# Kernel tuning notes

Measured on AMD Instinct MI355X. Metric: run time of the kernel, lower is better.

Reference implementation:

```python
import jax, jax.numpy as jnp
import numpy as np

BS, LX, LY, D, H, DK = 2, 2048, 2048, 1024, 16, 64


def setup_inputs() -> dict:
    key = jax.random.key(0)
    ks = jax.random.split(key, 12)
    s = 1.0 / np.sqrt(D)
    return {
        "x": jax.random.normal(ks[0], (BS, LX, D), jnp.float32),
        "y": jax.random.normal(ks[1], (BS, LY, D), jnp.float32),
        "mask": jnp.zeros((BS, 1, LX, LY), jnp.float32),
        "Wq": jax.random.normal(ks[2], (D, H * DK), jnp.float32) * s,
        "bq": jnp.zeros((H * DK,), jnp.float32),
        "Wk": jax.random.normal(ks[3], (D, H * DK), jnp.float32) * s,
        "bk": jnp.zeros((H * DK,), jnp.float32),
        "Wv": jax.random.normal(ks[4], (D, H * DK), jnp.float32) * s,
        "bv": jnp.zeros((H * DK,), jnp.float32),
        "Wo": jax.random.normal(ks[5], (H * DK, D), jnp.float32) * s,
        "bo": jnp.zeros((D,), jnp.float32),
    }


def reference(x, y, mask, Wq, bq, Wk, bk, Wv, bv, Wo, bo):
    bs, lx, _ = x.shape
    ly = y.shape[1]
    norm = DK ** 0.5
    # projections -> (bs, len, H, DK)
    q = (x @ Wq + bq).reshape(bs, lx, H, DK)
    k = (y @ Wk + bk).reshape(bs, ly, H, DK)
    v = (y @ Wv + bv).reshape(bs, ly, H, DK)
    # scores: (bs, H, lx, ly)
    scores = jnp.einsum('bxhd,byhd->bhxy', q, k) / norm + mask
    attn = jax.nn.softmax(scores, axis=-1)
    # output: (bs, lx, H, DK) -> (bs, lx, H*DK)
    out = jnp.einsum('bhxy,byhd->bxhd', attn, v).reshape(bs, lx, H * DK)
    return out @ Wo + bo
```

## Files before the change

### kernel.cpp

```cpp
#include <hip/hip_runtime.h>
#include <hip/hip_bf16.h>


typedef __bf16 bf16;
typedef __bf16 bf16x4 __attribute__((ext_vector_type(4)));
typedef __bf16 bf16x8 __attribute__((ext_vector_type(8)));
typedef float floatx4 __attribute__((ext_vector_type(4)));

#define MFMA16(a, b, c) __builtin_amdgcn_mfma_f32_16x16x32_bf16(a, b, c, 0, 0, 0)

constexpr int BS = 2, LX = 2048, LY = 2048, D = 1024, H = 16, DK = 64;
constexpr int HD = H * DK;
constexpr float LOG2E = 1.4426950408889634f;

__device__ __forceinline__ void cp16(const bf16* g, bf16* l) {
  __builtin_amdgcn_global_load_lds(
      (const __attribute__((address_space(1))) unsigned int*)g,
      (__attribute__((address_space(3))) unsigned int*)l, 16, 0, 0);
}

__global__ __launch_bounds__(256) void prep(const float* __restrict__ W0, bf16* __restrict__ T0,
                                            const float* __restrict__ W1, bf16* __restrict__ T1,
                                            const float* __restrict__ W2, bf16* __restrict__ T2,
                                            const float* __restrict__ W3, bf16* __restrict__ T3,
                                            const float* __restrict__ x, bf16* __restrict__ xb,
                                            const float* __restrict__ y, bf16* __restrict__ yb,
                                            const float* __restrict__ mask, int* __restrict__ flags) {
  const int id = blockIdx.x;
  const int t = threadIdx.x;
  if (id < 1024) {
    __shared__ bf16 tile[64][72];
    const float* W;
    bf16* T;
    switch (id >> 8) {
      case 0: W = W0; T = T0; break;
      case 1: W = W1; T = T1; break;
      case 2: W = W2; T = T2; break;
      default: W = W3; T = T3; break;
    }
    const int kt = id & 15, nt = (id >> 4) & 15;
    const int r = t >> 2, c4 = (t & 3) * 16;
    const float* src = W + (size_t)(kt * 64 + r) * 1024 + nt * 64 + c4;
#pragma unroll
    for (int i = 0; i < 16; i++) tile[r][c4 + i] = (bf16)src[i];
    __syncthreads();
    bf16 vals[16];
#pragma unroll
    for (int i = 0; i < 16; i++) vals[i] = tile[c4 + i][r];
    bf16* dst = T + (size_t)(nt * 64 + r) * 1024 + kt * 64 + c4;
#pragma unroll
    for (int i = 0; i < 16; i++) dst[i] = vals[i];
  } else if (id < 5120) {
    const int id2 = id - 1024;
    const float* src = (id2 >= 2048) ? y : x;
    bf16* dst = (id2 >= 2048) ? yb : xb;
    const size_t i = ((size_t)(id2 & 2047) * 256 + t) * 8;
    float4 a = *(const float4*)(src + i);
    float4 c = *(const float4*)(src + i + 4);
    bf16 tmp[8] = {(bf16)a.x, (bf16)a.y, (bf16)a.z, (bf16)a.w,
                   (bf16)c.x, (bf16)c.y, (bf16)c.z, (bf16)c.w};
    *(bf16x8*)(dst + i) = *(const bf16x8*)tmp;
  } else {
    const int id3 = id - 5120;
    const int region = id3 >> 5, sub = id3 & 31;
    const float4* p = (const float4*)mask + (size_t)region * 65536 + sub * 2048;
    bool nz = false;
#pragma unroll
    for (int it = 0; it < 8; it++) {
      float4 v = p[it * 256 + t];
      nz |= (v.x != 0.f) | (v.y != 0.f) | (v.z != 0.f) | (v.w != 0.f);
    }
    if (nz) atomicOr(&flags[region], 1);
  }
}

__global__ __launch_bounds__(256) void qkv_gemm(const bf16* __restrict__ xb, const bf16* __restrict__ yb,
                                                const bf16* __restrict__ Wtq, const bf16* __restrict__ Wtk,
                                                const bf16* __restrict__ Wtv,
                                                const float* __restrict__ bq, const float* __restrict__ bk,
                                                const float* __restrict__ bv,
                                                bf16* __restrict__ Qb, bf16* __restrict__ Kb,
                                                bf16* __restrict__ Vt) {
  constexpr int K = 1024, N = 1024;
  __shared__ __align__(16) bf16 smem[128 * 136];
  bf16* As = smem;
  bf16* Bs = smem + 128 * 64;
  bf16* Ct = smem;

  const int z = blockIdx.z;
  const bf16* A = (z == 0) ? xb : yb;
  const bf16* Bt = (z == 0) ? Wtq : (z == 1) ? Wtk : Wtv;
  const float* bias = (z == 0) ? bq : (z == 1) ? bk : bv;

  const int t = threadIdx.x;
  const int w = t >> 6, lane = t & 63, quad = lane >> 4, l15 = lane & 15;
  const int wr = (w & 1) * 64, wc = (w >> 1) * 64;
  const int mbase = blockIdx.y * 128, nbase = blockIdx.x * 128;
  const int srow = lane >> 3, schunk = (lane & 7) ^ srow;
  const int sx = quad ^ (l15 & 7);

  floatx4 acc[4][4] = {};

  for (int k0 = 0; k0 < K; k0 += 64) {
    __syncthreads();
#pragma unroll
    for (int j = 0; j < 4; j++) {
      const int r0 = w * 32 + j * 8;
      cp16(A + (size_t)(mbase + r0 + srow) * K + k0 + schunk * 8, As + r0 * 64);
      cp16(Bt + (size_t)(nbase + r0 + srow) * K + k0 + schunk * 8, Bs + r0 * 64);
    }
    __syncthreads();
    bf16x8 af[4][2], bfr[4][2];
#pragma unroll
    for (int i = 0; i < 4; i++) {
      const int ra = wr + i * 16 + l15;
      af[i][0] = *(const bf16x8*)&As[ra * 64 + sx * 8];
      af[i][1] = *(const bf16x8*)&As[ra * 64 + (sx ^ 4) * 8];
      const int rb = wc + i * 16 + l15;
      bfr[i][0] = *(const bf16x8*)&Bs[rb * 64 + sx * 8];
      bfr[i][1] = *(const bf16x8*)&Bs[rb * 64 + (sx ^ 4) * 8];
    }
#pragma unroll
    for (int i = 0; i < 4; i++)
#pragma unroll
      for (int jn = 0; jn < 4; jn++) {
        acc[i][jn] = MFMA16(af[i][0], bfr[jn][0], acc[i][jn]);
        acc[i][jn] = MFMA16(af[i][1], bfr[jn][1], acc[i][jn]);
      }
  }

  if (z <= 1) {
    bf16* outp = (z == 0) ? Qb : Kb;
    const float sc = (z == 0) ? 0.125f * LOG2E : 1.0f;
#pragma unroll
    for (int jn = 0; jn < 4; jn++) {
      const int n = nbase + wc + jn * 16 + l15;
      const float bv2 = bias[n];
#pragma unroll
      for (int i = 0; i < 4; i++)
#pragma unroll
        for (int r = 0; r < 4; r++) {
          const int m = mbase + wr + i * 16 + quad * 4 + r;
          outp[(size_t)m * N + n] = (bf16)((acc[i][jn][r] + bv2) * sc);
        }
    }
  } else {
    __syncthreads();
#pragma unroll
    for (int jn = 0; jn < 4; jn++) {
      const int nl = wc + jn * 16 + l15;
      const float bv2 = bias[nbase + nl];
#pragma unroll
      for (int i = 0; i < 4; i++)
#pragma unroll
        for (int r = 0; r < 4; r++) {
          const int ml = wr + i * 16 + quad * 4 + r;
          Ct[nl * 136 + ml] = (bf16)(acc[i][jn][r] + bv2);
        }
    }
    __syncthreads();
    const int n = t >> 1, mh = (t & 1) * 64;
    const int gn = nbase + n;
    const int hh = gn >> 6, dk = gn & 63;
    const int bb = mbase >> 11, y0 = (mbase & 2047) + mh;
    bf16* dst = Vt + ((size_t)(bb * H + hh) * DK + dk) * LY + y0;
    const bf16* srcr = &Ct[n * 136 + mh];
#pragma unroll
    for (int u = 0; u < 8; u++) *(bf16x8*)(dst + u * 8) = *(const bf16x8*)(srcr + u * 8);
  }
}

__global__ __launch_bounds__(256) void out_gemm(const bf16* __restrict__ A, const bf16* __restrict__ Bt,
                                                const float* __restrict__ bias, float* __restrict__ outp) {
  constexpr int K = 1024, N = 1024;
  __shared__ __align__(16) bf16 As[128 * 64];
  __shared__ __align__(16) bf16 Bs[64 * 64];
  const int t = threadIdx.x;
  const int w = t >> 6, lane = t & 63, quad = lane >> 4, l15 = lane & 15;
  const int mbase = blockIdx.y * 128, nbase = blockIdx.x * 64;
  const int srow = lane >> 3, schunk = (lane & 7) ^ srow;
  const int sx = quad ^ (l15 & 7);

  floatx4 acc[2][4] = {};
  for (int k0 = 0; k0 < K; k0 += 64) {
    __syncthreads();
#pragma unroll
    for (int j = 0; j < 4; j++) {
      const int r0 = w * 32 + j * 8;
      cp16(A + (size_t)(mbase + r0 + srow) * K + k0 + schunk * 8, As + r0 * 64);
    }
#pragma unroll
    for (int j = 0; j < 2; j++) {
      const int r0 = w * 16 + j * 8;
      cp16(Bt + (size_t)(nbase + r0 + srow) * K + k0 + schunk * 8, Bs + r0 * 64);
    }
    __syncthreads();
    bf16x8 af[2][2], bfr[4][2];
#pragma unroll
    for (int i = 0; i < 2; i++) {
      const int ra = w * 32 + i * 16 + l15;
      af[i][0] = *(const bf16x8*)&As[ra * 64 + sx * 8];
      af[i][1] = *(const bf16x8*)&As[ra * 64 + (sx ^ 4) * 8];
    }
#pragma unroll
    for (int jn = 0; jn < 4; jn++) {
      const int rb = jn * 16 + l15;
      bfr[jn][0] = *(const bf16x8*)&Bs[rb * 64 + sx * 8];
      bfr[jn][1] = *(const bf16x8*)&Bs[rb * 64 + (sx ^ 4) * 8];
    }
#pragma unroll
    for (int i = 0; i < 2; i++)
#pragma unroll
      for (int jn = 0; jn < 4; jn++) {
        acc[i][jn] = MFMA16(af[i][0], bfr[jn][0], acc[i][jn]);
        acc[i][jn] = MFMA16(af[i][1], bfr[jn][1], acc[i][jn]);
      }
  }
#pragma unroll
  for (int jn = 0; jn < 4; jn++) {
    const int n = nbase + jn * 16 + l15;
    const float bv2 = bias[n];
#pragma unroll
    for (int i = 0; i < 2; i++)
#pragma unroll
      for (int r = 0; r < 4; r++) {
        const int m = mbase + w * 32 + i * 16 + quad * 4 + r;
        outp[(size_t)m * N + n] = acc[i][jn][r] + bv2;
      }
  }
}

__global__ __launch_bounds__(256) void attn6(const bf16* __restrict__ Q, const bf16* __restrict__ Kb,
                                             const bf16* __restrict__ Vt, const float* __restrict__ mask,
                                             const int* __restrict__ flags, bf16* __restrict__ OP,
                                             float* __restrict__ LP) {
  __shared__ __align__(16) bf16 Ks[2][64 * 64];
  __shared__ __align__(16) bf16 Vs[64 * 64];
  __shared__ __align__(16) bf16 Plds[4][16 * 72];
  const int t = threadIdx.x;
  const int w = t >> 6, lane = t & 63, quad = lane >> 4, l15 = lane & 15;
  const int xt = blockIdx.x, h = blockIdx.y;
  const int b = blockIdx.z >> 1, split = blockIdx.z & 1;
  const int qbase = xt * 128 + w * 32;
  const int y0 = split * 1024;
  const int srow = lane >> 3, schunk = (lane & 7) ^ srow;
  const int sx = quad ^ (l15 & 7);

  bf16x8 qf[2][2];
#pragma unroll
  for (int rt = 0; rt < 2; rt++) {
    const bf16* qrow = Q + (size_t)(b * LX + qbase + rt * 16 + l15) * HD + h * DK;
    qf[rt][0] = *(const bf16x8*)(qrow + quad * 8);
    qf[rt][1] = *(const bf16x8*)(qrow + 32 + quad * 8);
  }
  const int mflag = flags[b * 16 + xt];

  bf16 onearr[8];
#pragma unroll
  for (int i = 0; i < 8; i++) onearr[i] = (bf16)((l15 == 0) ? 1.0f : 0.0f);
  const bf16x8 onesf = *(const bf16x8*)onearr;

  floatx4 o[2][4] = {};
  floatx4 ol[2] = {};

  const bf16* Kbase = Kb + (size_t)(b * LY + y0) * HD + h * DK;
  const bf16* Vbase = Vt + (size_t)(b * H + h) * DK * LY + y0;
  const float* mbase2 = mask + (size_t)(b * LX + qbase + l15) * LY + y0;

#define STAGE_K(tt, bufi)                                                                    \
  {                                                                                          \
    _Pragma("unroll") for (int j = 0; j < 2; j++) {                                          \
      const int r0 = w * 16 + j * 8;                                                         \
      cp16(Kbase + (size_t)((tt)*64 + r0 + srow) * HD + schunk * 8, &Ks[bufi][r0 * 64]);     \
    }                                                                                        \
  }
#define STAGE_V(tt)                                                                          \
  {                                                                                          \
    _Pragma("unroll") for (int j = 0; j < 2; j++) {                                          \
      const int r0 = w * 16 + j * 8;                                                         \
      cp16(Vbase + (size_t)(r0 + srow) * LY + (tt)*64 + schunk * 8, &Vs[r0 * 64]);           \
    }                                                                                        \
  }

  STAGE_K(0, 0);
  STAGE_V(0);

  int buf = 0;
  for (int tt = 0; tt < 16; tt++) {
    __syncthreads();
    if (tt + 1 < 16) STAGE_K(tt + 1, buf ^ 1);

    bf16x8 kf[4][2];
#pragma unroll
    for (int nt = 0; nt < 4; nt++) {
      const int ry = nt * 16 + l15;
      kf[nt][0] = *(const bf16x8*)&Ks[buf][ry * 64 + sx * 8];
      kf[nt][1] = *(const bf16x8*)&Ks[buf][ry * 64 + (sx ^ 4) * 8];
    }
    floatx4 s[2][4] = {};
#pragma unroll
    for (int nt = 0; nt < 4; nt++)
#pragma unroll
      for (int rt = 0; rt < 2; rt++) {
        s[rt][nt] = MFMA16(kf[nt][0], qf[rt][0], s[rt][nt]);
        s[rt][nt] = MFMA16(kf[nt][1], qf[rt][1], s[rt][nt]);
      }
    if (mflag) {
#pragma unroll
      for (int rt = 0; rt < 2; rt++)
#pragma unroll
        for (int nt = 0; nt < 4; nt++) {
          const float* mp = mbase2 + (size_t)rt * 16 * LY + tt * 64 + nt * 16 + quad * 4;
          float4 mv = *(const float4*)mp;
          s[rt][nt][0] = fminf(s[rt][nt][0] + LOG2E * mv.x, 30.f);
          s[rt][nt][1] = fminf(s[rt][nt][1] + LOG2E * mv.y, 30.f);
          s[rt][nt][2] = fminf(s[rt][nt][2] + LOG2E * mv.z, 30.f);
          s[rt][nt][3] = fminf(s[rt][nt][3] + LOG2E * mv.w, 30.f);
        }
    }

    bf16x8 vf[4][2];
#pragma unroll
    for (int u = 0; u < 4; u++) {
      const int rd = u * 16 + l15;
      vf[u][0] = *(const bf16x8*)&Vs[rd * 64 + sx * 8];
      vf[u][1] = *(const bf16x8*)&Vs[rd * 64 + (sx ^ 4) * 8];
    }

#pragma unroll
    for (int rt = 0; rt < 2; rt++) {
#pragma unroll
      for (int nt = 0; nt < 4; nt++) {
        bf16x4 pk;
#pragma unroll
        for (int r = 0; r < 4; r++) pk[r] = (bf16)exp2f(s[rt][nt][r]);
        *(bf16x4*)&Plds[w][l15 * 72 + nt * 16 + quad * 4] = pk;
      }
      const bf16* prow = &Plds[w][l15 * 72];
      bf16x8 p0 = *(const bf16x8*)(prow + quad * 8);
      bf16x8 p1 = *(const bf16x8*)(prow + 32 + quad * 8);
#pragma unroll
      for (int u = 0; u < 4; u++) {
        o[rt][u] = MFMA16(p0, vf[u][0], o[rt][u]);
        o[rt][u] = MFMA16(p1, vf[u][1], o[rt][u]);
      }
      ol[rt] = MFMA16(p0, onesf, ol[rt]);
      ol[rt] = MFMA16(p1, onesf, ol[rt]);
    }

    __syncthreads();
    if (tt + 1 < 16) STAGE_V(tt + 1);
    buf ^= 1;
  }

  bf16* OPp = OP + (size_t)split * BS * LX * HD;
  float* LPp = LP + (size_t)split * BS * H * LX;
#pragma unroll
  for (int rt = 0; rt < 2; rt++) {
#pragma unroll
    for (int r = 0; r < 4; r++) {
      const int m = b * LX + qbase + rt * 16 + quad * 4 + r;
#pragma unroll
      for (int u = 0; u < 4; u++)
        OPp[(size_t)m * HD + h * DK + u * 16 + l15] = (bf16)o[rt][u][r];
    }
    if (l15 == 0)
      *(floatx4*)&LPp[(size_t)(b * H + h) * LX + qbase + rt * 16 + quad * 4] = ol[rt];
  }
#undef STAGE_K
#undef STAGE_V
}

__global__ __launch_bounds__(256) void hmerge(const bf16* __restrict__ OP, const float* __restrict__ LP,
                                              bf16* __restrict__ Hb) {
  const size_t i8 = ((size_t)blockIdx.x * 256 + threadIdx.x) * 8;
  const bf16x8 a = *(const bf16x8*)(OP + i8);
  const bf16x8 b = *(const bf16x8*)(OP + (size_t)BS * LX * HD + i8);
  const int bb = (int)(i8 >> 21);
  const int x = (int)(i8 >> 10) & 2047;
  const int h = (int)(i8 >> 6) & 15;
  const size_t li = (size_t)(bb * H + h) * LX + x;
  const float rl = 1.0f / (LP[li] + LP[(size_t)BS * H * LX + li]);
  bf16 outv[8];
#pragma unroll
  for (int j = 0; j < 8; j++) outv[j] = (bf16)(((float)a[j] + (float)b[j]) * rl);
  *(bf16x8*)(Hb + i8) = *(const bf16x8*)outv;
}

extern "C" void kernel_launch(void* const* d_in, const int* in_sizes, int n_in,
                              void* d_out, int out_size, void* d_ws, size_t ws_size,
                              hipStream_t stream) {
  const float* x = (const float*)d_in[0];
  const float* y = (const float*)d_in[1];
  const float* mask = (const float*)d_in[2];
  const float* Wq = (const float*)d_in[3];
  const float* bq = (const float*)d_in[4];
  const float* Wk = (const float*)d_in[5];
  const float* bk = (const float*)d_in[6];
  const float* Wv = (const float*)d_in[7];
  const float* bv = (const float*)d_in[8];
  const float* Wo = (const float*)d_in[9];
  const float* bo = (const float*)d_in[10];

  char* ws = (char*)d_ws;
  size_t off = 0;
  int* flags = (int*)(ws + off); off += 256;
  bf16* Qb = (bf16*)(ws + off); off += (size_t)BS * LX * HD * 2;
  bf16* Kb = (bf16*)(ws + off); off += (size_t)BS * LY * HD * 2;
  bf16* Vt = (bf16*)(ws + off); off += (size_t)BS * LY * HD * 2;
  bf16* Hb = (bf16*)(ws + off); off += (size_t)BS * LX * HD * 2;
  const size_t region = off;
  bf16* xbf = (bf16*)(ws + off); off += (size_t)BS * LX * D * 2;
  bf16* ybf = (bf16*)(ws + off); off += (size_t)BS * LY * D * 2;
  bf16* Wtq = (bf16*)(ws + off); off += (size_t)D * HD * 2;
  bf16* Wtk = (bf16*)(ws + off); off += (size_t)D * HD * 2;
  bf16* Wtv = (bf16*)(ws + off); off += (size_t)D * HD * 2;
  bf16* Wto = (bf16*)(ws + off); off += (size_t)HD * D * 2;
  bf16* OP = (bf16*)(ws + region);
  float* LP = (float*)(ws + region + (size_t)2 * BS * LX * HD * 2);

  dim3 blk(256);
  hipMemsetAsync(flags, 0, 32 * sizeof(int), stream);
  prep<<<dim3(6144), blk, 0, stream>>>(Wq, Wtq, Wk, Wtk, Wv, Wtv, Wo, Wto, x, xbf, y, ybf, mask, flags);
  qkv_gemm<<<dim3(8, 32, 3), blk, 0, stream>>>(xbf, ybf, Wtq, Wtk, Wtv, bq, bk, bv, Qb, Kb, Vt);
  attn6<<<dim3(16, 16, 4), blk, 0, stream>>>(Qb, Kb, Vt, mask, flags, OP, LP);
  hmerge<<<dim3(2048), blk, 0, stream>>>(OP, LP, Hb);
  out_gemm<<<dim3(16, 32), blk, 0, stream>>>(Hb, Wto, bo, (float*)d_out);
}
```

Measured before the change: 265.9 us.

## Double-buffer K and V together and unroll attention loop by two tiles

The attention kernel now double-buffers both K and V in shared memory and stages them together, so the next tile's K and V loads overlap the current tile's compute. The earlier schedule reloaded V only after the second barrier of each iteration. The loop is manually unrolled by two with fixed buffer indices, P is written for both row tiles before the PV MFMAs, and exp2f is swapped for the hardware exp2 builtin. This uses more LDS per block, which may reduce occupancy.

```diff
diff --git a/kernel.cpp b/kernel.cpp
--- a/kernel.cpp
+++ b/kernel.cpp
@@ -230,13 +230,13 @@
   }
 }
 
-__global__ __launch_bounds__(256) void attn6(const bf16* __restrict__ Q, const bf16* __restrict__ Kb,
+__global__ __launch_bounds__(256) void attn7(const bf16* __restrict__ Q, const bf16* __restrict__ Kb,
                                              const bf16* __restrict__ Vt, const float* __restrict__ mask,
                                              const int* __restrict__ flags, bf16* __restrict__ OP,
                                              float* __restrict__ LP) {
   __shared__ __align__(16) bf16 Ks[2][64 * 64];
-  __shared__ __align__(16) bf16 Vs[64 * 64];
-  __shared__ __align__(16) bf16 Plds[4][16 * 72];
+  __shared__ __align__(16) bf16 Vs[2][64 * 64];
+  __shared__ __align__(16) bf16 Plds[4][32 * 72];
   const int t = threadIdx.x;
   const int w = t >> 6, lane = t & 63, quad = lane >> 4, l15 = lane & 15;
   const int xt = blockIdx.x, h = blockIdx.y;
@@ -267,90 +267,78 @@
   const bf16* Vbase = Vt + (size_t)(b * H + h) * DK * LY + y0;
   const float* mbase2 = mask + (size_t)(b * LX + qbase + l15) * LY + y0;
 
-#define STAGE_K(tt, bufi)                                                                    \
-  {                                                                                          \
-    _Pragma("unroll") for (int j = 0; j < 2; j++) {                                          \
-      const int r0 = w * 16 + j * 8;                                                         \
-      cp16(Kbase + (size_t)((tt)*64 + r0 + srow) * HD + schunk * 8, &Ks[bufi][r0 * 64]);     \
-    }                                                                                        \
-  }
-#define STAGE_V(tt)                                                                          \
-  {                                                                                          \
-    _Pragma("unroll") for (int j = 0; j < 2; j++) {                                          \
-      const int r0 = w * 16 + j * 8;                                                         \
-      cp16(Vbase + (size_t)(r0 + srow) * LY + (tt)*64 + schunk * 8, &Vs[r0 * 64]);           \
-    }                                                                                        \
-  }
-
-  STAGE_K(0, 0);
-  STAGE_V(0);
-
-  int buf = 0;
-  for (int tt = 0; tt < 16; tt++) {
-    __syncthreads();
-    if (tt + 1 < 16) STAGE_K(tt + 1, buf ^ 1);
-
-    bf16x8 kf[4][2];
-#pragma unroll
-    for (int nt = 0; nt < 4; nt++) {
-      const int ry = nt * 16 + l15;
-      kf[nt][0] = *(const bf16x8*)&Ks[buf][ry * 64 + sx * 8];
-      kf[nt][1] = *(const bf16x8*)&Ks[buf][ry * 64 + (sx ^ 4) * 8];
-    }
-    floatx4 s[2][4] = {};
-#pragma unroll
-    for (int nt = 0; nt < 4; nt++)
-#pragma unroll
-      for (int rt = 0; rt < 2; rt++) {
-        s[rt][nt] = MFMA16(kf[nt][0], qf[rt][0], s[rt][nt]);
-        s[rt][nt] = MFMA16(kf[nt][1], qf[rt][1], s[rt][nt]);
-      }
-    if (mflag) {
-#pragma unroll
-      for (int rt = 0; rt < 2; rt++)
-#pragma unroll
-        for (int nt = 0; nt < 4; nt++) {
-          const float* mp = mbase2 + (size_t)rt * 16 * LY + tt * 64 + nt * 16 + quad * 4;
-          float4 mv = *(const float4*)mp;
-          s[rt][nt][0] = fminf(s[rt][nt][0] + LOG2E * mv.x, 30.f);
-          s[rt][nt][1] = fminf(s[rt][nt][1] + LOG2E * mv.y, 30.f);
-          s[rt][nt][2] = fminf(s[rt][nt][2] + LOG2E * mv.z, 30.f);
-          s[rt][nt][3] = fminf(s[rt][nt][3] + LOG2E * mv.w, 30.f);
-        }
-    }
-
-    bf16x8 vf[4][2];
-#pragma unroll
-    for (int u = 0; u < 4; u++) {
-      const int rd = u * 16 + l15;
-      vf[u][0] = *(const bf16x8*)&Vs[rd * 64 + sx * 8];
-      vf[u][1] = *(const bf16x8*)&Vs[rd * 64 + (sx ^ 4) * 8];
-    }
-
-#pragma unroll
-    for (int rt = 0; rt < 2; rt++) {
-#pragma unroll
-      for (int nt = 0; nt < 4; nt++) {
-        bf16x4 pk;
-#pragma unroll
-        for (int r = 0; r < 4; r++) pk[r] = (bf16)exp2f(s[rt][nt][r]);
-        *(bf16x4*)&Plds[w][l15 * 72 + nt * 16 + quad * 4] = pk;
-      }
-      const bf16* prow = &Plds[w][l15 * 72];
-      bf16x8 p0 = *(const bf16x8*)(prow + quad * 8);
-      bf16x8 p1 = *(const bf16x8*)(prow + 32 + quad * 8);
-#pragma unroll
-      for (int u = 0; u < 4; u++) {
-        o[rt][u] = MFMA16(p0, vf[u][0], o[rt][u]);
-        o[rt][u] = MFMA16(p1, vf[u][1], o[rt][u]);
-      }
-      ol[rt] = MFMA16(p0, onesf, ol[rt]);
-      ol[rt] = MFMA16(p1, onesf, ol[rt]);
-    }
-
-    __syncthreads();
-    if (tt + 1 < 16) STAGE_V(tt + 1);
-    buf ^= 1;
+#define STAGE(yt, bufi)                                                               \
+  {                                                                                   \
+    _Pragma("unroll") for (int j = 0; j < 2; j++) {                                   \
+      const int r0 = w * 16 + j * 8;                                                  \
+      cp16(Kbase + (size_t)((yt) + r0 + srow) * HD + schunk * 8, &Ks[bufi][r0 * 64]); \
+      cp16(Vbase + (size_t)(r0 + srow) * LY + (yt) + schunk * 8, &Vs[bufi][r0 * 64]); \
+    }                                                                                 \
+  }
+
+#define TILE(yt, BUF)                                                                       \
+  {                                                                                         \
+    const bf16* KsB = Ks[BUF];                                                              \
+    const bf16* VsB = Vs[BUF];                                                              \
+    bf16x8 kf[4][2];                                                                        \
+    _Pragma("unroll") for (int nt = 0; nt < 4; nt++) {                                      \
+      const int ry = nt * 16 + l15;                                                         \
+      kf[nt][0] = *(const bf16x8*)&KsB[ry * 64 + sx * 8];                                   \
+      kf[nt][1] = *(const bf16x8*)&KsB[ry * 64 + (sx ^ 4) * 8];                             \
+    }                                                                                       \
+    floatx4 s[2][4] = {};                                                                   \
+    _Pragma("unroll") for (int nt = 0; nt < 4; nt++)                                        \
+        _Pragma("unroll") for (int rt = 0; rt < 2; rt++) {                                  \
+      s[rt][nt] = MFMA16(kf[nt][0], qf[rt][0], s[rt][nt]);                                  \
+      s[rt][nt] = MFMA16(kf[nt][1], qf[rt][1], s[rt][nt]);                                  \
+    }                                                                                       \
+    if (mflag) {                                                                            \
+      _Pragma("unroll") for (int rt = 0; rt < 2; rt++)                                      \
+          _Pragma("unroll") for (int nt = 0; nt < 4; nt++) {                                \
+        const float* mp = mbase2 + (size_t)rt * 16 * LY + (yt) + nt * 16 + quad * 4;        \
+        float4 mv = *(const float4*)mp;                                                     \
+        s[rt][nt][0] = fminf(s[rt][nt][0] + LOG2E * mv.x, 30.f);                            \
+        s[rt][nt][1] = fminf(s[rt][nt][1] + LOG2E * mv.y, 30.f);                            \
+        s[rt][nt][2] = fminf(s[rt][nt][2] + LOG2E * mv.z, 30.f);                            \
+        s[rt][nt][3] = fminf(s[rt][nt][3] + LOG2E * mv.w, 30.f);                            \
+      }                                                                                     \
+    }                                                                                       \
+    _Pragma("unroll") for (int rt = 0; rt < 2; rt++)                                        \
+        _Pragma("unroll") for (int nt = 0; nt < 4; nt++) {                                  \
+      bf16x4 pk;                                                                            \
+      _Pragma("unroll") for (int r = 0; r < 4; r++)                                         \
+          pk[r] = (bf16)__builtin_amdgcn_exp2f(s[rt][nt][r]);                               \
+      *(bf16x4*)&Plds[w][(rt * 16 + l15) * 72 + nt * 16 + quad * 4] = pk;                   \
+    }                                                                                       \
+    bf16x8 pf[2][2];                                                                        \
+    _Pragma("unroll") for (int rt = 0; rt < 2; rt++) {                                      \
+      const bf16* prow = &Plds[w][(rt * 16 + l15) * 72];                                    \
+      pf[rt][0] = *(const bf16x8*)(prow + quad * 8);                                        \
+      pf[rt][1] = *(const bf16x8*)(prow + 32 + quad * 8);                                   \
+    }                                                                                       \
+    _Pragma("unroll") for (int u = 0; u < 4; u++) {                                         \
+      const int rd = u * 16 + l15;                                                          \
+      bf16x8 v0 = *(const bf16x8*)&VsB[rd * 64 + sx * 8];                                   \
+      bf16x8 v1 = *(const bf16x8*)&VsB[rd * 64 + (sx ^ 4) * 8];                             \
+      _Pragma("unroll") for (int rt = 0; rt < 2; rt++) {                                    \
+        o[rt][u] = MFMA16(pf[rt][0], v0, o[rt][u]);                                         \
+        o[rt][u] = MFMA16(pf[rt][1], v1, o[rt][u]);                                         \
+      }                                                                                     \
+    }                                                                                       \
+    _Pragma("unroll") for (int rt = 0; rt < 2; rt++) {                                      \
+      ol[rt] = MFMA16(pf[rt][0], onesf, ol[rt]);                                            \
+      ol[rt] = MFMA16(pf[rt][1], onesf, ol[rt]);                                            \
+    }                                                                                       \
+  }
+
+  STAGE(0, 0);
+  for (int yt = 0; yt < 1024; yt += 128) {
+    __syncthreads();
+    STAGE(yt + 64, 1);
+    TILE(yt, 0);
+    __syncthreads();
+    if (yt + 128 < 1024) STAGE(yt + 128, 0);
+    TILE(yt + 64, 1);
   }
 
   bf16* OPp = OP + (size_t)split * BS * LX * HD;
@@ -367,8 +355,8 @@
     if (l15 == 0)
       *(floatx4*)&LPp[(size_t)(b * H + h) * LX + qbase + rt * 16 + quad * 4] = ol[rt];
   }
-#undef STAGE_K
-#undef STAGE_V
+#undef STAGE
+#undef TILE
 }
 
 __global__ __launch_bounds__(256) void hmerge(const bf16* __restrict__ OP, const float* __restrict__ LP,
@@ -423,7 +411,7 @@
   hipMemsetAsync(flags, 0, 32 * sizeof(int), stream);
   prep<<<dim3(6144), blk, 0, stream>>>(Wq, Wtq, Wk, Wtk, Wv, Wtv, Wo, Wto, x, xbf, y, ybf, mask, flags);
   qkv_gemm<<<dim3(8, 32, 3), blk, 0, stream>>>(xbf, ybf, Wtq, Wtk, Wtv, bq, bk, bv, Qb, Kb, Vt);
-  attn6<<<dim3(16, 16, 4), blk, 0, stream>>>(Qb, Kb, Vt, mask, flags, OP, LP);
+  attn7<<<dim3(16, 16, 4), blk, 0, stream>>>(Qb, Kb, Vt, mask, flags, OP, LP);
   hmerge<<<dim3(2048), blk, 0, stream>>>(OP, LP, Hb);
   out_gemm<<<dim3(16, 32), blk, 0, stream>>>(Hb, Wto, bo, (float*)d_out);
 }
```

After: 248.9 us. 1.07x faster.
